# Optimization experiments

Measured on AMD Instinct MI355X. Metric: run time of the kernel, lower is better.

Reference implementation:

```python
import jax, jax.numpy as jnp
import numpy as np

N_R = 768; N_L = 768; D_IN = 20; H = 250
H1 = 1024; H2 = 512; H3 = 256; OUT = 2


def setup_inputs() -> dict:
    key = jax.random.key(0)
    ks = jax.random.split(key, 16)
    s = 0.05
    def rn(k, shape):
        return jax.random.normal(k, shape, jnp.float32) * s
    return {
        "v_r": rn(ks[0], (N_R, D_IN)),
        "v_l": rn(ks[1], (N_L, D_IN)),
        # 2-layer bidirectional LSTM params, stacked over direction [2, ...]
        # bias = b_ih + b_hh fused into a single term per direction.
        "w_ih0": rn(ks[2], (2, 4 * H, D_IN)),
        "w_hh0": rn(ks[3], (2, 4 * H, H)),
        "b0":    rn(ks[4], (2, 4 * H)),
        "w_ih1": rn(ks[5], (2, 4 * H, 2 * H)),
        "w_hh1": rn(ks[6], (2, 4 * H, H)),
        "b1":    rn(ks[7], (2, 4 * H)),
        "W1": rn(ks[8], (H1, 2 * H)),  "b_1": rn(ks[9], (H1,)),
        "W2": rn(ks[10], (H2, H1)),    "b_2": rn(ks[11], (H2,)),
        "W3": rn(ks[12], (H3, 2 * H2)), "b_3": rn(ks[13], (H3,)),
        "Wo": rn(ks[14], (OUT, H3)),   "b_o": rn(ks[15], (OUT,)),
    }


def _lstm_dir(x, Wih, Whh, b):
    # x: [T, D]; gate order i,f,g,o as in torch nn.LSTM
    Hd = Whh.shape[1]
    xz = x @ Wih.T + b  # precompute input projection [T, 4H]
    def step(carry, z_in):
        h, c = carry
        z = z_in + h @ Whh.T
        i, f, g, o = jnp.split(z, 4)
        i = jax.nn.sigmoid(i); f = jax.nn.sigmoid(f)
        g = jnp.tanh(g);       o = jax.nn.sigmoid(o)
        c = f * c + i * g
        h = o * jnp.tanh(c)
        return (h, c), h
    h0 = jnp.zeros((Hd,), x.dtype)
    _, hs = jax.lax.scan(step, (h0, h0), xz)
    return hs  # [T, H]


def _bilstm(x, wih, whh, b):
    fwd = _lstm_dir(x, wih[0], whh[0], b[0])
    bwd = _lstm_dir(x[::-1], wih[1], whh[1], b[1])[::-1]
    return jnp.concatenate([fwd, bwd], axis=-1)  # [T, 2H]


def _encode(x, w_ih0, w_hh0, b0, w_ih1, w_hh1, b1, W1, b_1, W2, b_2):
    h = _bilstm(x, w_ih0, w_hh0, b0)   # layer 0
    h = _bilstm(h, w_ih1, w_hh1, b1)   # layer 1 (inter-layer dropout = identity in eval)
    h = jax.nn.relu(h @ W1.T + b_1)    # [T, H1]
    h = jax.nn.relu(h @ W2.T + b_2)    # [T, H2]
    return h


def reference(v_r, v_l, w_ih0, w_hh0, b0, w_ih1, w_hh1, b1,
              W1, b_1, W2, b_2, W3, b_3, Wo, b_o):
    r2 = _encode(v_r, w_ih0, w_hh0, b0, w_ih1, w_hh1, b1, W1, b_1, W2, b_2)  # [N_r, H2]
    l2 = _encode(v_l, w_ih0, w_hh0, b0, w_ih1, w_hh1, b1, W1, b_1, W2, b_2)  # [N_l, H2]
    # Pairwise concat [r2[i]; l2[j]] @ W3.T  ==  r2 @ W3[:, :H2].T  +  l2 @ W3[:, H2:].T
    # (avoids materializing the [N_r*N_l, 2*H2] concat the torch loop builds)
    d = r2.shape[1]
    pr = r2 @ W3[:, :d].T          # [N_r, H3]
    pl = l2 @ W3[:, d:].T          # [N_l, H3]
    h3 = jax.nn.relu(pr[:, None, :] + pl[None, :, :] + b_3)  # [N_r, N_l, H3]
    h3 = h3.reshape(-1, h3.shape[-1])                        # [N_r*N_l, H3]
    logits = h3 @ Wo.T + b_o                                 # [N_r*N_l, 2]
    return jax.nn.log_softmax(logits, axis=-1)
```

## Files before the change

kernel.cpp:

```cpp
#include <hip/hip_runtime.h>
#include <hip/hip_bf16.h>

#ifndef __has_builtin
#define __has_builtin(x) 0
#endif
#if __has_builtin(__builtin_amdgcn_fdot2)
#define HAVE_FDOT2 1
#else
#define HAVE_FDOT2 0
#endif

typedef _Float16 f16x2 __attribute__((ext_vector_type(2)));
typedef _Float16 f16x8 __attribute__((ext_vector_type(8)));
typedef float float4v __attribute__((ext_vector_type(4)));
typedef float float2v __attribute__((ext_vector_type(2)));

__device__ __forceinline__ void dot2acc(f16x2 w, f16x2 h, float& acc) {
#if HAVE_FDOT2
    acc = __builtin_amdgcn_fdot2(w, h, acc, false);
#else
    acc = fmaf((float)w.x, (float)h.x, fmaf((float)w.y, (float)h.y, acc));
#endif
}

__device__ __forceinline__ f16x2 pk(float a, float b) {
    f16x2 v; v.x = (_Float16)a; v.y = (_Float16)b; return v;
}

__device__ __forceinline__ void barrier_lgkm() {
    asm volatile("s_waitcnt lgkmcnt(0)\n\ts_barrier" ::: "memory");
}

#define TT 768
#define DIN 20
#define HH 250
#define H4 1000

#define OFF_BUFA 0
#define OFF_HCAT0 3072000
#define OFF_HCAT1 3840000

__global__ __launch_bounds__(256) void k_xz0(
    const float* __restrict__ vr, const float* __restrict__ vl,
    const float* __restrict__ wih0, const float* __restrict__ b0,
    float* __restrict__ xz0)
{
    int t = blockIdx.x;
    int c = blockIdx.y;
    int s = c >> 1, d = c & 1;
    const float* x = (s ? vl : vr) + t * DIN;
    __shared__ float xs[DIN];
    if (threadIdx.x < DIN) xs[threadIdx.x] = x[threadIdx.x];
    __syncthreads();
    const float* W  = wih0 + (long)d * H4 * DIN;
    const float* bb = b0 + d * H4;
    for (int g = threadIdx.x; g < H4; g += 256) {
        const float* wr = W + g * DIN;
        float z = bb[g];
#pragma unroll
        for (int k = 0; k < DIN; ++k) z = fmaf(wr[k], xs[k], z);
        xz0[((long)c * TT + t) * H4 + g] = z;
    }
}

__global__ __launch_bounds__(512)
__attribute__((amdgpu_waves_per_eu(2, 2)))
void k_lstm(
    const float* __restrict__ xz,
    const float* __restrict__ whh,
    float* __restrict__ hcat)
{
    __shared__ __align__(16) _Float16 hh[256];
    __shared__ float zF[256];
    __shared__ float zO[256];
    __shared__ float wlds[15000];

    int c = blockIdx.x;
    int s = c >> 1, d = c & 1;
    int t = threadIdx.x;
    int tr = (t < 500) ? t : 499;

    f16x2 wA[125];
    f16x2 wB[96];
    {
        const float* pA = whh + ((long)d * H4 + tr) * HH;
        const float* pB = whh + ((long)d * H4 + tr + 500) * HH;
#pragma unroll
        for (int i = 0; i < 125; ++i) wA[i] = pk(pA[2 * i], pA[2 * i + 1]);
#pragma unroll
        for (int i = 0; i < 96; ++i) wB[i] = pk(pB[2 * i], pB[2 * i + 1]);
        if (t < 500) {
#pragma unroll
            for (int i = 0; i < 29; ++i)
                wlds[t * 30 + i] =
                    __builtin_bit_cast(float, pk(pB[192 + 2 * i], pB[193 + 2 * i]));
        }
    }
    if (t < 256) hh[t] = (_Float16)0.f;
    __syncthreads();

    const float* xzc = xz + (long)c * TT * H4;
    float* hout = hcat + (long)s * TT * 500 + d * HH;
    const float* myw = &wlds[tr * 30];
    float cst = 0.f;

    for (int tau = 0; tau < TT; ++tau) {
        int trow = d ? (TT - 1 - tau) : tau;
        float zA = xzc[(long)trow * H4 + tr];
        float zB = xzc[(long)trow * H4 + tr + 500];

        float a0 = 0.f, a1 = 0.f, a2 = 0.f, a3 = 0.f;
        float b0 = 0.f, b1 = 0.f, b2 = 0.f, b3 = 0.f;
#pragma unroll
        for (int b = 0; b < 24; ++b) {
            f16x8 hv = *(const f16x8*)(&hh[8 * b]);
            f16x2 h0 = __builtin_shufflevector(hv, hv, 0, 1);
            f16x2 h1 = __builtin_shufflevector(hv, hv, 2, 3);
            f16x2 h2 = __builtin_shufflevector(hv, hv, 4, 5);
            f16x2 h3 = __builtin_shufflevector(hv, hv, 6, 7);
            dot2acc(wA[4 * b],     h0, a0);
            dot2acc(wA[4 * b + 1], h1, a1);
            dot2acc(wA[4 * b + 2], h2, a2);
            dot2acc(wA[4 * b + 3], h3, a3);
            dot2acc(wB[4 * b],     h0, b0);
            dot2acc(wB[4 * b + 1], h1, b1);
            dot2acc(wB[4 * b + 2], h2, b2);
            dot2acc(wB[4 * b + 3], h3, b3);
        }
#pragma unroll
        for (int b = 0; b < 7; ++b) {
            f16x8 hv = *(const f16x8*)(&hh[192 + 8 * b]);
            float2v w01 = *(const float2v*)(&myw[4 * b]);
            float2v w23 = *(const float2v*)(&myw[4 * b + 2]);
            f16x2 h0 = __builtin_shufflevector(hv, hv, 0, 1);
            f16x2 h1 = __builtin_shufflevector(hv, hv, 2, 3);
            f16x2 h2 = __builtin_shufflevector(hv, hv, 4, 5);
            f16x2 h3 = __builtin_shufflevector(hv, hv, 6, 7);
            dot2acc(wA[96 + 4 * b],     h0, a0);
            dot2acc(wA[96 + 4 * b + 1], h1, a1);
            dot2acc(wA[96 + 4 * b + 2], h2, a2);
            dot2acc(wA[96 + 4 * b + 3], h3, a3);
            dot2acc(__builtin_bit_cast(f16x2, w01.x), h0, b0);
            dot2acc(__builtin_bit_cast(f16x2, w01.y), h1, b1);
            dot2acc(__builtin_bit_cast(f16x2, w23.x), h2, b2);
            dot2acc(__builtin_bit_cast(f16x2, w23.y), h3, b3);
        }
        {
            f16x2 hl = *(const f16x2*)(&hh[248]);
            dot2acc(wA[124], hl, a0);
            dot2acc(__builtin_bit_cast(f16x2, myw[28]), hl, b0);
        }
        float zAt = zA + (a0 + a1) + (a2 + a3);
        float zBt = zB + (b0 + b1) + (b2 + b3);

        if (t >= 250 && t < 500) { zF[t - 250] = zAt; zO[t - 250] = zBt; }
        barrier_lgkm();
        if (t < 250) {
            float zi = zAt, zf = zF[t], zg = zBt, zo = zO[t];
            float ig = 1.f / (1.f + __expf(-zi));
            float fg = 1.f / (1.f + __expf(-zf));
            float gg = tanhf(zg);
            float og = 1.f / (1.f + __expf(-zo));
            cst = fg * cst + ig * gg;
            float h = og * tanhf(cst);
            hout[(long)trow * 500 + t] = h;
            hh[t] = (_Float16)h;
        }
        barrier_lgkm();
    }
}

__global__ __launch_bounds__(256) void k_gemm(
    const float* __restrict__ A, long sA, int aDiv,
    const float* __restrict__ B, long sB, int bMod, int ldb,
    const float* __restrict__ bias, long sBias,
    float* __restrict__ C, long sC,
    int M, int N, int K, int relu)
{
    int bz = blockIdx.z;
    A += (long)(bz / aDiv) * sA;
    B += (long)(bz % bMod) * sB;
    if (bias) bias += (long)(bz % bMod) * sBias;
    C += (long)bz * sC;

    __shared__ float As[16][68];
    __shared__ float Bs[16][68];
    int n0 = blockIdx.x * 64, m0 = blockIdx.y * 64;
    int tid = threadIdx.x;
    int tn = tid % 16, tm = tid / 16;
    int lr = tid / 4;
    int lk4 = (tid % 4) * 4;
    float acc[4][4] = {};

    for (int k0 = 0; k0 < K; k0 += 16) {
        const float* Ap = A + (long)(m0 + lr) * K + k0 + lk4;
        const float* Bp = B + (long)(n0 + lr) * ldb + k0 + lk4;
        bool nok = (n0 + lr) < N;
#pragma unroll
        for (int j = 0; j < 4; ++j) {
            int kk = k0 + lk4 + j;
            As[lk4 + j][lr] = (kk < K) ? Ap[j] : 0.f;
            Bs[lk4 + j][lr] = (nok && kk < K) ? Bp[j] : 0.f;
        }
        __syncthreads();
#pragma unroll
        for (int kk = 0; kk < 16; ++kk) {
            float a4[4], b4[4];
#pragma unroll
            for (int i = 0; i < 4; ++i) a4[i] = As[kk][tm * 4 + i];
#pragma unroll
            for (int i = 0; i < 4; ++i) b4[i] = Bs[kk][tn * 4 + i];
#pragma unroll
            for (int i = 0; i < 4; ++i)
#pragma unroll
                for (int j = 0; j < 4; ++j)
                    acc[i][j] = fmaf(a4[i], b4[j], acc[i][j]);
        }
        __syncthreads();
    }
#pragma unroll
    for (int j = 0; j < 4; ++j) {
        int n = n0 + tn * 4 + j;
        if (n >= N) continue;
        float bv = bias ? bias[n] : 0.f;
#pragma unroll
        for (int i = 0; i < 4; ++i) {
            int m = m0 + tm * 4 + i;
            float v = acc[i][j] + bv;
            if (relu) v = fmaxf(v, 0.f);
            C[(long)m * N + n] = v;
        }
    }
}

__global__ __launch_bounds__(256) void k_pair(
    const float* __restrict__ pr, const float* __restrict__ pl,
    const float* __restrict__ b3,
    const float* __restrict__ Wo,
    const float* __restrict__ bo,
    float* __restrict__ out)
{
    __shared__ float prs[8][257];
    __shared__ float pls[32][257];
    __shared__ float b3s[256], wo0[256], wo1[256];
    int i0 = blockIdx.x * 8, j0 = blockIdx.y * 32;
    int tid = threadIdx.x;
    for (int idx = tid; idx < 8 * 256; idx += 256)
        prs[idx >> 8][idx & 255] = pr[(long)(i0 + (idx >> 8)) * 256 + (idx & 255)];
    for (int idx = tid; idx < 32 * 256; idx += 256)
        pls[idx >> 8][idx & 255] = pl[(long)(j0 + (idx >> 8)) * 256 + (idx & 255)];
    {
        b3s[tid] = b3[tid];
        wo0[tid] = Wo[tid];
        wo1[tid] = Wo[256 + tid];
    }
    __syncthreads();
    int il = tid >> 5, jl = tid & 31;
    float a0 = 0.f, a1 = 0.f;
#pragma unroll 8
    for (int k = 0; k < 256; ++k) {
        float h = prs[il][k] + pls[jl][k] + b3s[k];
        h = fmaxf(h, 0.f);
        a0 = fmaf(h, wo0[k], a0);
        a1 = fmaf(h, wo1[k], a1);
    }
    a0 += bo[0];
    a1 += bo[1];
    float m = fmaxf(a0, a1);
    float lse = m + __logf(__expf(a0 - m) + __expf(a1 - m));
    long p = ((long)(i0 + il) * TT + (j0 + jl)) * 2;
    out[p]     = a0 - lse;
    out[p + 1] = a1 - lse;
}

extern "C" void kernel_launch(void* const* d_in, const int* in_sizes, int n_in,
                              void* d_out, int out_size, void* d_ws, size_t ws_size,
                              hipStream_t stream) {
    const float* vr    = (const float*)d_in[0];
    const float* vl    = (const float*)d_in[1];
    const float* wih0  = (const float*)d_in[2];
    const float* whh0  = (const float*)d_in[3];
    const float* b0    = (const float*)d_in[4];
    const float* wih1  = (const float*)d_in[5];
    const float* whh1  = (const float*)d_in[6];
    const float* b1    = (const float*)d_in[7];
    const float* W1    = (const float*)d_in[8];
    const float* b_1   = (const float*)d_in[9];
    const float* W2    = (const float*)d_in[10];
    const float* b_2   = (const float*)d_in[11];
    const float* W3    = (const float*)d_in[12];
    const float* b_3   = (const float*)d_in[13];
    const float* Wo    = (const float*)d_in[14];
    const float* b_o   = (const float*)d_in[15];
    float* out = (float*)d_out;

    float* wsf   = (float*)d_ws;
    float* bufA  = wsf + OFF_BUFA;
    float* hcat0 = wsf + OFF_HCAT0;
    float* hcat1 = wsf + OFF_HCAT1;
    float* e1 = bufA;
    float* e2 = bufA + 1572864;
    float* pr = bufA + 2359296;
    float* pl = bufA + 2555904;

    k_xz0<<<dim3(TT, 4, 1), 256, 0, stream>>>(vr, vl, wih0, b0, bufA);
    k_lstm<<<4, 512, 0, stream>>>(bufA, whh0, hcat0);
    k_gemm<<<dim3(16, 12, 4), 256, 0, stream>>>(hcat0, 384000L, 2,
                                                wih1, 500000L, 2, 500,
                                                b1, 1000L,
                                                bufA, 768000L, TT, 1000, 500, 0);
    k_lstm<<<4, 512, 0, stream>>>(bufA, whh1, hcat1);
    k_gemm<<<dim3(16, 12, 2), 256, 0, stream>>>(hcat1, 384000L, 1,
                                                W1, 0L, 1, 500,
                                                b_1, 0L,
                                                e1, 786432L, TT, 1024, 500, 1);
    k_gemm<<<dim3(8, 12, 2), 256, 0, stream>>>(e1, 786432L, 1,
                                               W2, 0L, 1, 1024,
                                               b_2, 0L,
                                               e2, 393216L, TT, 512, 1024, 1);
    k_gemm<<<dim3(4, 12, 2), 256, 0, stream>>>(e2, 393216L, 1,
                                               W3, 512L, 2, 1024,
                                               (const float*)nullptr, 0L,
                                               pr, 196608L, TT, 256, 512, 0);
    k_pair<<<dim3(96, 24, 1), 256, 0, stream>>>(pr, pl, b_3, Wo, b_o, out);
}
```

Before: 3.134 ms.

## Restructure LSTM recurrence to one thread per hidden unit with double-buffered h

```diff
diff --git a/kernel.cpp b/kernel.cpp
--- a/kernel.cpp
+++ b/kernel.cpp
@@ -63,109 +63,129 @@
     }
 }
 
-__global__ __launch_bounds__(512)
-__attribute__((amdgpu_waves_per_eu(2, 2)))
-void k_lstm(
+__global__ __launch_bounds__(256, 1) void k_lstm(
     const float* __restrict__ xz,
     const float* __restrict__ whh,
     float* __restrict__ hcat)
 {
-    __shared__ __align__(16) _Float16 hh[256];
-    __shared__ float zF[256];
-    __shared__ float zO[256];
-    __shared__ float wlds[15000];
+    __shared__ __align__(16) _Float16 hbuf[2][256];
+    __shared__ float wlds[250 * 64];
 
     int c = blockIdx.x;
     int s = c >> 1, d = c & 1;
     int t = threadIdx.x;
-    int tr = (t < 500) ? t : 499;
-
-    f16x2 wA[125];
-    f16x2 wB[96];
+    int u = (t < 250) ? t : 249;
+
+    f16x2 wi[125], wf[125], wg[125], wo[64];
     {
-        const float* pA = whh + ((long)d * H4 + tr) * HH;
-        const float* pB = whh + ((long)d * H4 + tr + 500) * HH;
-#pragma unroll
-        for (int i = 0; i < 125; ++i) wA[i] = pk(pA[2 * i], pA[2 * i + 1]);
-#pragma unroll
-        for (int i = 0; i < 96; ++i) wB[i] = pk(pB[2 * i], pB[2 * i + 1]);
-        if (t < 500) {
-#pragma unroll
-            for (int i = 0; i < 29; ++i)
-                wlds[t * 30 + i] =
-                    __builtin_bit_cast(float, pk(pB[192 + 2 * i], pB[193 + 2 * i]));
-        }
-    }
-    if (t < 256) hh[t] = (_Float16)0.f;
+        const float* pi = whh + ((long)d * H4 + u) * HH;
+        const float* pf = whh + ((long)d * H4 + 250 + u) * HH;
+        const float* pg = whh + ((long)d * H4 + 500 + u) * HH;
+        const float* po = whh + ((long)d * H4 + 750 + u) * HH;
+#pragma unroll
+        for (int i = 0; i < 125; ++i) wi[i] = pk(pi[2 * i], pi[2 * i + 1]);
+#pragma unroll
+        for (int i = 0; i < 125; ++i) wf[i] = pk(pf[2 * i], pf[2 * i + 1]);
+#pragma unroll
+        for (int i = 0; i < 125; ++i) wg[i] = pk(pg[2 * i], pg[2 * i + 1]);
+#pragma unroll
+        for (int i = 0; i < 64; ++i) wo[i] = pk(po[2 * i], po[2 * i + 1]);
+        if (t < 250) {
+            int base = t << 6;
+#pragma unroll
+            for (int i = 0; i < 61; ++i) {
+                int cm = i >> 2;
+                int pos = (((cm ^ (t & 7)) << 2) | (i & 3));
+                wlds[base + pos] =
+                    __builtin_bit_cast(float, pk(po[2 * (64 + i)], po[2 * (64 + i) + 1]));
+            }
+        }
+    }
+    hbuf[0][t] = (_Float16)0.f;
+    hbuf[1][t] = (_Float16)0.f;
     __syncthreads();
 
     const float* xzc = xz + (long)c * TT * H4;
     float* hout = hcat + (long)s * TT * 500 + d * HH;
-    const float* myw = &wlds[tr * 30];
+    int wbase = u << 6;
+    int usw = u & 7;
     float cst = 0.f;
 
     for (int tau = 0; tau < TT; ++tau) {
         int trow = d ? (TT - 1 - tau) : tau;
-        float zA = xzc[(long)trow * H4 + tr];
-        float zB = xzc[(long)trow * H4 + tr + 500];
-
-        float a0 = 0.f, a1 = 0.f, a2 = 0.f, a3 = 0.f;
-        float b0 = 0.f, b1 = 0.f, b2 = 0.f, b3 = 0.f;
-#pragma unroll
-        for (int b = 0; b < 24; ++b) {
-            f16x8 hv = *(const f16x8*)(&hh[8 * b]);
-            f16x2 h0 = __builtin_shufflevector(hv, hv, 0, 1);
-            f16x2 h1 = __builtin_shufflevector(hv, hv, 2, 3);
-            f16x2 h2 = __builtin_shufflevector(hv, hv, 4, 5);
-            f16x2 h3 = __builtin_shufflevector(hv, hv, 6, 7);
-            dot2acc(wA[4 * b],     h0, a0);
-            dot2acc(wA[4 * b + 1], h1, a1);
-            dot2acc(wA[4 * b + 2], h2, a2);
-            dot2acc(wA[4 * b + 3], h3, a3);
-            dot2acc(wB[4 * b],     h0, b0);
-            dot2acc(wB[4 * b + 1], h1, b1);
-            dot2acc(wB[4 * b + 2], h2, b2);
-            dot2acc(wB[4 * b + 3], h3, b3);
-        }
-#pragma unroll
-        for (int b = 0; b < 7; ++b) {
-            f16x8 hv = *(const f16x8*)(&hh[192 + 8 * b]);
-            float2v w01 = *(const float2v*)(&myw[4 * b]);
-            float2v w23 = *(const float2v*)(&myw[4 * b + 2]);
-            f16x2 h0 = __builtin_shufflevector(hv, hv, 0, 1);
-            f16x2 h1 = __builtin_shufflevector(hv, hv, 2, 3);
-            f16x2 h2 = __builtin_shufflevector(hv, hv, 4, 5);
-            f16x2 h3 = __builtin_shufflevector(hv, hv, 6, 7);
-            dot2acc(wA[96 + 4 * b],     h0, a0);
-            dot2acc(wA[96 + 4 * b + 1], h1, a1);
-            dot2acc(wA[96 + 4 * b + 2], h2, a2);
-            dot2acc(wA[96 + 4 * b + 3], h3, a3);
-            dot2acc(__builtin_bit_cast(f16x2, w01.x), h0, b0);
-            dot2acc(__builtin_bit_cast(f16x2, w01.y), h1, b1);
-            dot2acc(__builtin_bit_cast(f16x2, w23.x), h2, b2);
-            dot2acc(__builtin_bit_cast(f16x2, w23.y), h3, b3);
+        const float* xr = xzc + (long)trow * H4;
+        float zi0 = xr[u];
+        float zf0 = xr[250 + u];
+        float zg0 = xr[500 + u];
+        float zo0 = xr[750 + u];
+
+        f16x8 hv = *(const f16x8*)(&hbuf[tau & 1][8 * (t & 31)]);
+        int hd[4];
+        hd[0] = __builtin_bit_cast(int, (f16x2)__builtin_shufflevector(hv, hv, 0, 1));
+        hd[1] = __builtin_bit_cast(int, (f16x2)__builtin_shufflevector(hv, hv, 2, 3));
+        hd[2] = __builtin_bit_cast(int, (f16x2)__builtin_shufflevector(hv, hv, 4, 5));
+        hd[3] = __builtin_bit_cast(int, (f16x2)__builtin_shufflevector(hv, hv, 6, 7));
+
+        float ai[4] = {0.f, 0.f, 0.f, 0.f};
+        float af[4] = {0.f, 0.f, 0.f, 0.f};
+        float ag[4] = {0.f, 0.f, 0.f, 0.f};
+        float ao[4] = {0.f, 0.f, 0.f, 0.f};
+
+#define HPAIR(p) __builtin_bit_cast(f16x2, __builtin_amdgcn_readlane(hd[(p) & 3], (p) >> 2))
+#define DOT4(p, WO2, AIDX) do {                     \
+            f16x2 h2_ = HPAIR(p);                   \
+            dot2acc(wi[p], h2_, ai[(p) & 3]);       \
+            dot2acc(wf[p], h2_, af[(p) & 3]);       \
+            dot2acc(wg[p], h2_, ag[(p) & 3]);       \
+            dot2acc((WO2), h2_, ao[AIDX]);          \
+        } while (0)
+
+#pragma unroll
+        for (int k = 0; k < 8; ++k) {
+#pragma unroll
+            for (int j = 0; j < 8; ++j) {
+                int p = 8 * k + j;
+                DOT4(p, wo[p], p & 3);
+            }
+        }
+#pragma unroll
+        for (int k = 8; k < 15; ++k) {
+            float4v w01 = *(const float4v*)(&wlds[wbase + (((2 * k - 16) ^ usw) << 2)]);
+            float4v w23 = *(const float4v*)(&wlds[wbase + (((2 * k - 15) ^ usw) << 2)]);
+            DOT4(8 * k + 0, __builtin_bit_cast(f16x2, w01.x), 0);
+            DOT4(8 * k + 1, __builtin_bit_cast(f16x2, w01.y), 1);
+            DOT4(8 * k + 2, __builtin_bit_cast(f16x2, w01.z), 2);
+            DOT4(8 * k + 3, __builtin_bit_cast(f16x2, w01.w), 3);
+            DOT4(8 * k + 4, __builtin_bit_cast(f16x2, w23.x), 0);
+            DOT4(8 * k + 5, __builtin_bit_cast(f16x2, w23.y), 1);
+            DOT4(8 * k + 6, __builtin_bit_cast(f16x2, w23.z), 2);
+            DOT4(8 * k + 7, __builtin_bit_cast(f16x2, w23.w), 3);
         }
         {
-            f16x2 hl = *(const f16x2*)(&hh[248]);
-            dot2acc(wA[124], hl, a0);
-            dot2acc(__builtin_bit_cast(f16x2, myw[28]), hl, b0);
-        }
-        float zAt = zA + (a0 + a1) + (a2 + a3);
-        float zBt = zB + (b0 + b1) + (b2 + b3);
-
-        if (t >= 250 && t < 500) { zF[t - 250] = zAt; zO[t - 250] = zBt; }
-        barrier_lgkm();
-        if (t < 250) {
-            float zi = zAt, zf = zF[t], zg = zBt, zo = zO[t];
-            float ig = 1.f / (1.f + __expf(-zi));
-            float fg = 1.f / (1.f + __expf(-zf));
-            float gg = tanhf(zg);
-            float og = 1.f / (1.f + __expf(-zo));
-            cst = fg * cst + ig * gg;
-            float h = og * tanhf(cst);
-            hout[(long)trow * 500 + t] = h;
-            hh[t] = (_Float16)h;
-        }
+            float4v wt = *(const float4v*)(&wlds[wbase + ((14 ^ usw) << 2)]);
+            float wlast = wlds[wbase + ((15 ^ usw) << 2)];
+            DOT4(120, __builtin_bit_cast(f16x2, wt.x), 0);
+            DOT4(121, __builtin_bit_cast(f16x2, wt.y), 1);
+            DOT4(122, __builtin_bit_cast(f16x2, wt.z), 2);
+            DOT4(123, __builtin_bit_cast(f16x2, wt.w), 3);
+            DOT4(124, __builtin_bit_cast(f16x2, wlast), 0);
+        }
+#undef DOT4
+#undef HPAIR
+
+        float zi = zi0 + (ai[0] + ai[1]) + (ai[2] + ai[3]);
+        float zf = zf0 + (af[0] + af[1]) + (af[2] + af[3]);
+        float zg = zg0 + (ag[0] + ag[1]) + (ag[2] + ag[3]);
+        float zo = zo0 + (ao[0] + ao[1]) + (ao[2] + ao[3]);
+
+        float ig = 1.f / (1.f + __expf(-zi));
+        float fg = 1.f / (1.f + __expf(-zf));
+        float gg = tanhf(zg);
+        float og = 1.f / (1.f + __expf(-zo));
+        cst = fg * cst + ig * gg;
+        float h = og * tanhf(cst);
+        hout[(long)trow * 500 + u] = h;
+        hbuf[(tau & 1) ^ 1][u] = (_Float16)h;
         barrier_lgkm();
     }
 }
@@ -304,12 +324,12 @@
     float* pl = bufA + 2555904;
 
     k_xz0<<<dim3(TT, 4, 1), 256, 0, stream>>>(vr, vl, wih0, b0, bufA);
-    k_lstm<<<4, 512, 0, stream>>>(bufA, whh0, hcat0);
+    k_lstm<<<4, 256, 0, stream>>>(bufA, whh0, hcat0);
     k_gemm<<<dim3(16, 12, 4), 256, 0, stream>>>(hcat0, 384000L, 2,
                                                 wih1, 500000L, 2, 500,
                                                 b1, 1000L,
                                                 bufA, 768000L, TT, 1000, 500, 0);
-    k_lstm<<<4, 512, 0, stream>>>(bufA, whh1, hcat1);
+    k_lstm<<<4, 256, 0, stream>>>(bufA, whh1, hcat1);
     k_gemm<<<dim3(16, 12, 2), 256, 0, stream>>>(hcat1, 384000L, 1,
                                                 W1, 0L, 1, 500,
                                                 b_1, 0L,
```

Result: slower. 6.566 ms (+109.5%).
